# Optimization experiments

Measured on AMD Instinct MI355X. Metric: run time of the kernel, lower is better.

## Reference

```python
import jax, jax.numpy as jnp
import numpy as np

B, SQ, SK, DQ, DK, DV = 8, 2048, 2048, 128, 128, 128

def setup_inputs() -> dict:
    key = jax.random.key(0)
    k1, k2, k3, k4 = jax.random.split(key, 4)
    # xavier_uniform for weights [DQ, DK]
    limit = float(np.sqrt(6.0 / (DQ + DK)))
    weights = jax.random.uniform(k4, (DQ, DK), jnp.float32, -limit, limit)
    return {
        "query": jax.random.normal(k1, (B, SQ, DQ), jnp.float32),
        "key": jax.random.normal(k2, (B, SK, DK), jnp.float32),
        "value": jax.random.normal(k3, (B, SK, DV), jnp.float32),
        "weights": weights,
    }

def reference(query, key, value, weights):
    # score = (query @ W) @ key^T, computed as two GEMMs (faithful math, no [B,Sq,Dk,Sk] blow-up)
    qw = jnp.einsum('bqd,dk->bqk', query, weights)          # [B,SQ,DK]
    score = jnp.einsum('bqk,bsk->bqs', qw, key)             # [B,SQ,SK]
    weight = jax.nn.softmax(score, axis=-1)                 # dropout=0 -> identity
    out = jnp.einsum('bqs,bsv->bqv', weight, value)         # [B,SQ,DV]
    return out, weight
```

## Files before the change

kernel.cpp:

```cpp
#include <hip/hip_runtime.h>

#define B_  8
#define SQ_ 2048
#define SK_ 2048
#define D_  128

typedef float  f32x4 __attribute__((ext_vector_type(4)));
typedef short  s16x8 __attribute__((ext_vector_type(8)));
typedef __bf16 b16x8 __attribute__((ext_vector_type(8)));

__device__ __forceinline__ f32x4 mfma16(s16x8 a, s16x8 b, f32x4 c) {
    return __builtin_amdgcn_mfma_f32_16x16x32_bf16(
        __builtin_bit_cast(b16x8, a), __builtin_bit_cast(b16x8, b), c, 0, 0, 0);
}

__device__ __forceinline__ unsigned int bfpack(float a, float b) {
    return (__float_as_uint(a) >> 16) | (__float_as_uint(b) & 0xFFFF0000u);
}

__device__ __forceinline__ void split4(const float4 v, uint2& hi, uint2& lo) {
    float hx = __uint_as_float(__float_as_uint(v.x) & 0xFFFF0000u);
    float hy = __uint_as_float(__float_as_uint(v.y) & 0xFFFF0000u);
    float hz = __uint_as_float(__float_as_uint(v.z) & 0xFFFF0000u);
    float hw = __uint_as_float(__float_as_uint(v.w) & 0xFFFF0000u);
    hi.x = bfpack(v.x, v.y); hi.y = bfpack(v.z, v.w);
    lo.x = bfpack(v.x - hx, v.y - hy); lo.y = bfpack(v.z - hz, v.w - hw);
}

union U8 { unsigned int u[4]; s16x8 v; };

__global__ __launch_bounds__(256) void k1_qw(const float* __restrict__ q,
                                             const float* __restrict__ w,
                                             float* __restrict__ qw) {
    __shared__ float Ws[D_ * D_];
    const int tid = threadIdx.x;
    const int rowbase = blockIdx.x * 64;
    #pragma unroll
    for (int t = 0; t < 16; ++t) {
        int i4 = t * 256 + tid;
        ((float4*)Ws)[i4] = ((const float4*)w)[i4];
    }
    __syncthreads();
    const int mg = tid >> 4, cg = tid & 15;
    const int c0 = cg * 8;
    const float* qrow[4];
    #pragma unroll
    for (int i = 0; i < 4; ++i)
        qrow[i] = q + (size_t)(rowbase + mg * 4 + i) * D_;
    float acc[4][8];
    #pragma unroll
    for (int i = 0; i < 4; ++i)
        #pragma unroll
        for (int j = 0; j < 8; ++j) acc[i][j] = 0.0f;
    for (int d0 = 0; d0 < D_; d0 += 16) {
        float qr[4][16];
        #pragma unroll
        for (int i = 0; i < 4; ++i)
            #pragma unroll
            for (int c4 = 0; c4 < 4; ++c4)
                *(float4*)&qr[i][c4 * 4] = *(const float4*)(qrow[i] + d0 + c4 * 4);
        #pragma unroll
        for (int dd = 0; dd < 16; ++dd) {
            const int d = d0 + dd;
            float4 w0 = *(const float4*)&Ws[d * D_ + c0];
            float4 w1 = *(const float4*)&Ws[d * D_ + c0 + 4];
            #pragma unroll
            for (int i = 0; i < 4; ++i) {
                float a = qr[i][dd];
                acc[i][0] += a * w0.x; acc[i][1] += a * w0.y;
                acc[i][2] += a * w0.z; acc[i][3] += a * w0.w;
                acc[i][4] += a * w1.x; acc[i][5] += a * w1.y;
                acc[i][6] += a * w1.z; acc[i][7] += a * w1.w;
            }
        }
    }
    #pragma unroll
    for (int i = 0; i < 4; ++i) {
        float* dst = qw + (size_t)(rowbase + mg * 4 + i) * D_ + c0;
        *(float4*)dst       = make_float4(acc[i][0], acc[i][1], acc[i][2], acc[i][3]);
        *(float4*)(dst + 4) = make_float4(acc[i][4], acc[i][5], acc[i][6], acc[i][7]);
    }
}

__global__ __launch_bounds__(256) void k2_score(
        const float* __restrict__ qw, const float* __restrict__ key,
        float* __restrict__ S) {
    __shared__ unsigned short Khi[64 * 136];
    __shared__ unsigned short Klo[64 * 136];

    const int tid  = threadIdx.x;
    const int b    = blockIdx.z;
    const int m0   = blockIdx.y * 64;
    const int n0   = blockIdx.x * 64;
    const int w    = tid >> 6, lane = tid & 63;
    const int mw   = w >> 1,  nw   = w & 1;
    const int quad = lane >> 4, l15 = lane & 15;

    #pragma unroll
    for (int it = 0; it < 8; ++it) {
        int idx = it * 256 + tid;
        int r = idx >> 5, c4 = idx & 31;
        float4 v = ((const float4*)(key + ((size_t)b * SK_ + n0 + r) * D_))[c4];
        uint2 h, l; split4(v, h, l);
        unsigned int* ph = (unsigned int*)Khi + r * 68 + c4 * 2;
        unsigned int* pl = (unsigned int*)Klo + r * 68 + c4 * 2;
        ph[0] = h.x; ph[1] = h.y; pl[0] = l.x; pl[1] = l.y;
    }

    s16x8 a_hi[2][4], a_lo[2][4];
    #pragma unroll
    for (int rt = 0; rt < 2; ++rt) {
        const float* ar = qw + ((size_t)b * SQ_ + m0 + mw * 32 + rt * 16 + l15) * D_;
        #pragma unroll
        for (int k0 = 0; k0 < 4; ++k0) {
            const float* p = ar + k0 * 32 + quad * 8;
            float4 v0 = *(const float4*)p;
            float4 v1 = *(const float4*)(p + 4);
            uint2 h0, l0, h1, l1;
            split4(v0, h0, l0); split4(v1, h1, l1);
            U8 H, L;
            H.u[0] = h0.x; H.u[1] = h0.y; H.u[2] = h1.x; H.u[3] = h1.y;
            L.u[0] = l0.x; L.u[1] = l0.y; L.u[2] = l1.x; L.u[3] = l1.y;
            a_hi[rt][k0] = H.v; a_lo[rt][k0] = L.v;
        }
    }
    __syncthreads();

    f32x4 acc[2][2];
    #pragma unroll
    for (int rt = 0; rt < 2; ++rt)
        #pragma unroll
        for (int ct = 0; ct < 2; ++ct) acc[rt][ct] = (f32x4){0.f, 0.f, 0.f, 0.f};

    #pragma unroll
    for (int k0 = 0; k0 < 4; ++k0) {
        const int c8 = (k0 * 4 + quad) * 8;
        s16x8 bh[2], bl[2];
        #pragma unroll
        for (int ct = 0; ct < 2; ++ct) {
            int rb = nw * 32 + ct * 16 + l15;
            bh[ct] = *(const s16x8*)&Khi[rb * 136 + c8];
            bl[ct] = *(const s16x8*)&Klo[rb * 136 + c8];
        }
        #pragma unroll
        for (int rt = 0; rt < 2; ++rt)
            #pragma unroll
            for (int ct = 0; ct < 2; ++ct) {
                acc[rt][ct] = mfma16(a_hi[rt][k0], bh[ct], acc[rt][ct]);
                acc[rt][ct] = mfma16(a_lo[rt][k0], bh[ct], acc[rt][ct]);
                acc[rt][ct] = mfma16(a_hi[rt][k0], bl[ct], acc[rt][ct]);
            }
    }

    #pragma unroll
    for (int rt = 0; rt < 2; ++rt) {
        float* Sp = S + ((size_t)b * SQ_ + m0 + mw * 32 + rt * 16 + quad * 4) * SK_
                      + n0 + nw * 32 + l15;
        #pragma unroll
        for (int r = 0; r < 4; ++r)
            #pragma unroll
            for (int ct = 0; ct < 2; ++ct)
                Sp[(size_t)r * SK_ + ct * 16] = acc[rt][ct][r];
    }
}

__global__ __launch_bounds__(256) void k2b_stats(const float* __restrict__ S,
        float* __restrict__ m_ws, float* __restrict__ l_ws) {
    const int row  = blockIdx.x * 4 + (threadIdx.x >> 6);
    const int lane = threadIdx.x & 63;
    const float4* p = (const float4*)(S + (size_t)row * SK_);
    float4 x[8];
    #pragma unroll
    for (int i = 0; i < 8; ++i) x[i] = p[i * 64 + lane];

    float m = -1e30f;
    #pragma unroll
    for (int i = 0; i < 8; ++i)
        m = fmaxf(m, fmaxf(fmaxf(x[i].x, x[i].y), fmaxf(x[i].z, x[i].w)));
    #pragma unroll
    for (int off = 32; off; off >>= 1) m = fmaxf(m, __shfl_xor(m, off, 64));

    float s = 0.f;
    #pragma unroll
    for (int i = 0; i < 8; ++i)
        s += __expf(x[i].x - m) + __expf(x[i].y - m) +
             __expf(x[i].z - m) + __expf(x[i].w - m);
    #pragma unroll
    for (int off = 32; off; off >>= 1) s += __shfl_xor(s, off, 64);

    if (lane == 0) {
        m_ws[row] = m;
        l_ws[row] = s;
    }
}

__global__ __launch_bounds__(256) void k3_pv(float* __restrict__ Wgt,
        const float* __restrict__ V, float* __restrict__ O,
        const float* __restrict__ m_ws, const float* __restrict__ l_ws) {
    __shared__ unsigned short Pt[16 * 72];
    __shared__ unsigned short Vt[128 * 72];

    const int tid  = threadIdx.x;
    const int b    = blockIdx.y;
    const int m0   = blockIdx.x * 16;
    const int w    = tid >> 6, lane = tid & 63;
    const int quad = lane >> 4, l15 = lane & 15;

    const int pr = tid >> 4, pc = tid & 15;
    const float m_r  = m_ws[(size_t)b * SQ_ + m0 + pr];
    const float invl = 1.0f / l_ws[(size_t)b * SQ_ + m0 + pr];
    float* Prow = Wgt + ((size_t)b * SQ_ + m0 + pr) * SK_;

    const int vn4 = tid >> 3, vk2 = tid & 7;
    const float* Vb = V + (size_t)b * SK_ * D_;

    f32x4 acc[2];
    acc[0] = (f32x4){0.f, 0.f, 0.f, 0.f};
    acc[1] = (f32x4){0.f, 0.f, 0.f, 0.f};

    for (int kt = 0; kt < SK_; kt += 64) {
        __syncthreads();
        {
            float4 s4 = ((const float4*)(Prow + kt))[pc];
            float4 p4;
            p4.x = __expf(s4.x - m_r) * invl;
            p4.y = __expf(s4.y - m_r) * invl;
            p4.z = __expf(s4.z - m_r) * invl;
            p4.w = __expf(s4.w - m_r) * invl;
            ((float4*)(Prow + kt))[pc] = p4;
            unsigned int* pp = (unsigned int*)Pt + pr * 36 + pc * 2;
            pp[0] = bfpack(p4.x, p4.y);
            pp[1] = bfpack(p4.z, p4.w);
        }
        #pragma unroll
        for (int i = 0; i < 4; ++i) {
            int kp = vk2 * 4 + i;
            const float* vp = Vb + (size_t)(kt + kp * 2) * D_ + vn4 * 4;
            float4 va  = *(const float4*)vp;
            float4 vb4 = *(const float4*)(vp + D_);
            unsigned int* qv = (unsigned int*)Vt;
            qv[(vn4 * 4 + 0) * 36 + kp] = bfpack(va.x, vb4.x);
            qv[(vn4 * 4 + 1) * 36 + kp] = bfpack(va.y, vb4.y);
            qv[(vn4 * 4 + 2) * 36 + kp] = bfpack(va.z, vb4.z);
            qv[(vn4 * 4 + 3) * 36 + kp] = bfpack(va.w, vb4.w);
        }
        __syncthreads();
        #pragma unroll
        for (int k0 = 0; k0 < 2; ++k0) {
            int c8 = (k0 * 4 + quad) * 8;
            s16x8 af = *(const s16x8*)&Pt[l15 * 72 + c8];
            #pragma unroll
            for (int nf = 0; nf < 2; ++nf) {
                s16x8 bf = *(const s16x8*)&Vt[(w * 32 + nf * 16 + l15) * 72 + c8];
                acc[nf] = mfma16(af, bf, acc[nf]);
            }
        }
    }

    float* Op = O + ((size_t)b * SQ_ + m0 + quad * 4) * D_ + w * 32 + l15;
    #pragma unroll
    for (int nf = 0; nf < 2; ++nf)
        #pragma unroll
        for (int r = 0; r < 4; ++r)
            Op[(size_t)r * D_ + nf * 16] = acc[nf][r];
}

extern "C" void kernel_launch(void* const* d_in, const int* in_sizes, int n_in,
                              void* d_out, int out_size, void* d_ws, size_t ws_size,
                              hipStream_t stream) {
    const float* q = (const float*)d_in[0];
    const float* k = (const float*)d_in[1];
    const float* v = (const float*)d_in[2];
    const float* w = (const float*)d_in[3];
    float* out    = (float*)d_out;
    float* weight = out + (size_t)B_ * SQ_ * D_;
    float* qw     = out;
    float* m_ws   = (float*)d_ws;
    float* l_ws   = m_ws + (size_t)B_ * SQ_;

    k1_qw<<<(B_ * SQ_) / 64, 256, 0, stream>>>(q, w, qw);
    k2_score<<<dim3(SK_ / 64, SQ_ / 64, B_), 256, 0, stream>>>(qw, k, weight);
    k2b_stats<<<(B_ * SQ_) / 4, 256, 0, stream>>>(weight, m_ws, l_ws);
    k3_pv<<<dim3(SQ_ / 16, B_), 256, 0, stream>>>(weight, v, out, m_ws, l_ws);
}
```

Baseline: 383.4 us.

## Replace materialized score matrix with two-pass recompute: stats kernel plus fused softmax-PV

Removes the separate score, stats and PV kernels. A split-K stats kernel recomputes Q·K^T in registers and keeps an online max and sum, with no full score matrix written. A fused kernel then recomputes the scores, writes the normalized weights once, and accumulates P·V through LDS atomics across four K-split waves. Q·W is now stored pre-split into bf16 hi/lo in the output buffer. This avoids writing the score matrix, reading it back, and rewriting it, at the cost of computing Q·K^T twice and loading K and V straight from global memory with strided, uncached-in-LDS access.

Result: slower. 542.8 us (+41.6%).

```diff
diff --git a/kernel.cpp b/kernel.cpp
--- a/kernel.cpp
+++ b/kernel.cpp
@@ -1,18 +1,35 @@
 #include <hip/hip_runtime.h>
 
-#define B_  8
-#define SQ_ 2048
-#define SK_ 2048
-#define D_  128
+#define B_   8
+#define SQ_  2048
+#define SK_  2048
+#define D_   128
+#define KSPLIT_ 4
+#define KRANGE_ (SK_ / KSPLIT_)
+#define NSTEP_  (KRANGE_ / 16)
+#define BSQ_ (B_ * SQ_)
 
 typedef float  f32x4 __attribute__((ext_vector_type(4)));
 typedef short  s16x8 __attribute__((ext_vector_type(8)));
+typedef short  s16x4 __attribute__((ext_vector_type(4)));
 typedef __bf16 b16x8 __attribute__((ext_vector_type(8)));
 
-__device__ __forceinline__ f32x4 mfma16(s16x8 a, s16x8 b, f32x4 c) {
+__device__ __forceinline__ f32x4 mfma_k32(s16x8 a, s16x8 b, f32x4 c) {
     return __builtin_amdgcn_mfma_f32_16x16x32_bf16(
         __builtin_bit_cast(b16x8, a), __builtin_bit_cast(b16x8, b), c, 0, 0, 0);
 }
+
+#if __has_builtin(__builtin_amdgcn_mfma_f32_16x16x16bf16_1k)
+__device__ __forceinline__ f32x4 mfma_k16(s16x4 a, s16x4 b, f32x4 c) {
+    return __builtin_amdgcn_mfma_f32_16x16x16bf16_1k(a, b, c, 0, 0, 0);
+}
+#else
+__device__ __forceinline__ f32x4 mfma_k16(s16x4 a, s16x4 b, f32x4 c) {
+    f32x4 d;
+    asm("v_mfma_f32_16x16x16_bf16 %0, %1, %2, %3" : "=v"(d) : "v"(a), "v"(b), "v"(c));
+    return d;
+}
+#endif
 
 __device__ __forceinline__ unsigned int bfpack(float a, float b) {
     return (__float_as_uint(a) >> 16) | (__float_as_uint(b) & 0xFFFF0000u);
@@ -28,10 +45,32 @@
 }
 
 union U8 { unsigned int u[4]; s16x8 v; };
+union U4 { unsigned int u[2]; s16x4 v; };
+
+__device__ __forceinline__ f32x4 qk_tile(const float* __restrict__ kr,
+                                         const s16x8* q_hi, const s16x8* q_lo,
+                                         int quad) {
+    f32x4 acc = (f32x4){0.f, 0.f, 0.f, 0.f};
+    #pragma unroll
+    for (int dc = 0; dc < 4; ++dc) {
+        const float* p = kr + dc * 32 + quad * 8;
+        float4 v0 = *(const float4*)p;
+        float4 v1 = *(const float4*)(p + 4);
+        uint2 h0, l0, h1, l1;
+        split4(v0, h0, l0); split4(v1, h1, l1);
+        U8 H, L;
+        H.u[0] = h0.x; H.u[1] = h0.y; H.u[2] = h1.x; H.u[3] = h1.y;
+        L.u[0] = l0.x; L.u[1] = l0.y; L.u[2] = l1.x; L.u[3] = l1.y;
+        acc = mfma_k32(H.v, q_hi[dc], acc);
+        acc = mfma_k32(L.v, q_hi[dc], acc);
+        acc = mfma_k32(H.v, q_lo[dc], acc);
+    }
+    return acc;
+}
 
 __global__ __launch_bounds__(256) void k1_qw(const float* __restrict__ q,
                                              const float* __restrict__ w,
-                                             float* __restrict__ qw) {
+                                             unsigned int* __restrict__ qwp) {
     __shared__ float Ws[D_ * D_];
     const int tid = threadIdx.x;
     const int rowbase = blockIdx.x * 64;
@@ -76,193 +115,138 @@
     }
     #pragma unroll
     for (int i = 0; i < 4; ++i) {
-        float* dst = qw + (size_t)(rowbase + mg * 4 + i) * D_ + c0;
-        *(float4*)dst       = make_float4(acc[i][0], acc[i][1], acc[i][2], acc[i][3]);
-        *(float4*)(dst + 4) = make_float4(acc[i][4], acc[i][5], acc[i][6], acc[i][7]);
-    }
-}
-
-__global__ __launch_bounds__(256) void k2_score(
-        const float* __restrict__ qw, const float* __restrict__ key,
-        float* __restrict__ S) {
-    __shared__ unsigned short Khi[64 * 136];
-    __shared__ unsigned short Klo[64 * 136];
-
+        float4 v0 = make_float4(acc[i][0], acc[i][1], acc[i][2], acc[i][3]);
+        float4 v1 = make_float4(acc[i][4], acc[i][5], acc[i][6], acc[i][7]);
+        uint2 h0, l0, h1, l1;
+        split4(v0, h0, l0); split4(v1, h1, l1);
+        unsigned int* dst = qwp + (size_t)(rowbase + mg * 4 + i) * 128;
+        *(uint4*)(dst + cg * 4)      = make_uint4(h0.x, h0.y, h1.x, h1.y);
+        *(uint4*)(dst + 64 + cg * 4) = make_uint4(l0.x, l0.y, l1.x, l1.y);
+    }
+}
+
+__global__ __launch_bounds__(256, 4) void k_stats(
+        const unsigned short* __restrict__ qwp, const float* __restrict__ key,
+        float* __restrict__ mp, float* __restrict__ lp) {
+    const int blk  = ((int)blockIdx.x & 7) * 128 + ((int)blockIdx.x >> 3);
+    const int wid  = blk * 4 + (threadIdx.x >> 6);
+    const int lane = threadIdx.x & 63;
+    const int quad = lane >> 4, l15 = lane & 15;
+    const int qb = wid & 127;
+    const int ks = (wid >> 7) & 3;
+    const int b  = wid >> 9;
+
+    const unsigned short* qrow = qwp + ((size_t)b * SQ_ + qb * 16 + l15) * 256;
+    s16x8 q_hi[4], q_lo[4];
+    #pragma unroll
+    for (int dc = 0; dc < 4; ++dc) {
+        q_hi[dc] = *(const s16x8*)(qrow + dc * 32 + quad * 8);
+        q_lo[dc] = *(const s16x8*)(qrow + 128 + dc * 32 + quad * 8);
+    }
+
+    const float* Kb = key + ((size_t)b * SK_ + ks * KRANGE_) * D_;
+    float m_run = -3.0e38f, l_run = 0.f;
+    for (int st = 0; st < NSTEP_; ++st) {
+        const float* kr = Kb + (size_t)(st * 16 + l15) * D_;
+        f32x4 acc = qk_tile(kr, q_hi, q_lo, quad);
+        float t = fmaxf(fmaxf(acc[0], acc[1]), fmaxf(acc[2], acc[3]));
+        float mn = fmaxf(m_run, t);
+        l_run = l_run * __expf(m_run - mn)
+              + __expf(acc[0] - mn) + __expf(acc[1] - mn)
+              + __expf(acc[2] - mn) + __expf(acc[3] - mn);
+        m_run = mn;
+    }
+    #pragma unroll
+    for (int off = 16; off <= 32; off <<= 1) {
+        float om = __shfl_xor(m_run, off, 64);
+        float ol = __shfl_xor(l_run, off, 64);
+        float mn = fmaxf(m_run, om);
+        l_run = l_run * __expf(m_run - mn) + ol * __expf(om - mn);
+        m_run = mn;
+    }
+    if (lane < 16) {
+        size_t row = (size_t)b * SQ_ + qb * 16 + l15;
+        mp[(size_t)ks * BSQ_ + row] = m_run;
+        lp[(size_t)ks * BSQ_ + row] = l_run;
+    }
+}
+
+__global__ __launch_bounds__(512, 4) void k_fused(
+        const unsigned short* qwp, const float* __restrict__ key,
+        const float* __restrict__ val, float* out, float* __restrict__ wgt,
+        const float* __restrict__ mp, const float* __restrict__ lp) {
+    __shared__ float Ot[32][132];
     const int tid  = threadIdx.x;
-    const int b    = blockIdx.z;
-    const int m0   = blockIdx.y * 64;
-    const int n0   = blockIdx.x * 64;
-    const int w    = tid >> 6, lane = tid & 63;
-    const int mw   = w >> 1,  nw   = w & 1;
-    const int quad = lane >> 4, l15 = lane & 15;
-
-    #pragma unroll
-    for (int it = 0; it < 8; ++it) {
-        int idx = it * 256 + tid;
-        int r = idx >> 5, c4 = idx & 31;
-        float4 v = ((const float4*)(key + ((size_t)b * SK_ + n0 + r) * D_))[c4];
-        uint2 h, l; split4(v, h, l);
-        unsigned int* ph = (unsigned int*)Khi + r * 68 + c4 * 2;
-        unsigned int* pl = (unsigned int*)Klo + r * 68 + c4 * 2;
-        ph[0] = h.x; ph[1] = h.y; pl[0] = l.x; pl[1] = l.y;
-    }
-
-    s16x8 a_hi[2][4], a_lo[2][4];
-    #pragma unroll
-    for (int rt = 0; rt < 2; ++rt) {
-        const float* ar = qw + ((size_t)b * SQ_ + m0 + mw * 32 + rt * 16 + l15) * D_;
-        #pragma unroll
-        for (int k0 = 0; k0 < 4; ++k0) {
-            const float* p = ar + k0 * 32 + quad * 8;
-            float4 v0 = *(const float4*)p;
-            float4 v1 = *(const float4*)(p + 4);
-            uint2 h0, l0, h1, l1;
-            split4(v0, h0, l0); split4(v1, h1, l1);
-            U8 H, L;
-            H.u[0] = h0.x; H.u[1] = h0.y; H.u[2] = h1.x; H.u[3] = h1.y;
-            L.u[0] = l0.x; L.u[1] = l0.y; L.u[2] = l1.x; L.u[3] = l1.y;
-            a_hi[rt][k0] = H.v; a_lo[rt][k0] = L.v;
+    const int blk  = ((int)blockIdx.x & 7) * 64 + ((int)blockIdx.x >> 3);
+    const int wv   = tid >> 6;
+    const int qg   = wv >> 2;
+    const int ks   = wv & 3;
+    const int lane = tid & 63, quad = lane >> 4, l15 = lane & 15;
+    const int b  = blk >> 6;
+    const int qb = (blk & 63) * 2 + qg;
+
+    for (int i = tid; i < 32 * 132; i += 512) ((float*)Ot)[i] = 0.f;
+    __syncthreads();
+
+    const unsigned short* qrow = qwp + ((size_t)b * SQ_ + qb * 16 + l15) * 256;
+    s16x8 q_hi[4], q_lo[4];
+    #pragma unroll
+    for (int dc = 0; dc < 4; ++dc) {
+        q_hi[dc] = *(const s16x8*)(qrow + dc * 32 + quad * 8);
+        q_lo[dc] = *(const s16x8*)(qrow + 128 + dc * 32 + quad * 8);
+    }
+
+    const size_t row = (size_t)b * SQ_ + qb * 16 + l15;
+    float mf = -3.0e38f, lf = 0.f;
+    #pragma unroll
+    for (int s = 0; s < KSPLIT_; ++s) {
+        float ms = mp[(size_t)s * BSQ_ + row];
+        float ls = lp[(size_t)s * BSQ_ + row];
+        float mn = fmaxf(mf, ms);
+        lf = lf * __expf(mf - mn) + ls * __expf(ms - mn);
+        mf = mn;
+    }
+    const float linv = 1.0f / lf;
+
+    const float* Kb = key + ((size_t)b * SK_ + ks * KRANGE_) * D_;
+    const float* Vb = val + ((size_t)b * SK_ + ks * KRANGE_) * D_;
+    float* Wp = wgt + row * SK_ + ks * KRANGE_ + quad * 4;
+
+    f32x4 acc_o[8];
+    #pragma unroll
+    for (int i = 0; i < 8; ++i) acc_o[i] = (f32x4){0.f, 0.f, 0.f, 0.f};
+
+    for (int st = 0; st < NSTEP_; ++st) {
+        const float* kr = Kb + (size_t)(st * 16 + l15) * D_;
+        f32x4 s4 = qk_tile(kr, q_hi, q_lo, quad);
+        f32x4 p;
+        #pragma unroll
+        for (int r = 0; r < 4; ++r) p[r] = __expf(s4[r] - mf) * linv;
+        *(float4*)(Wp + st * 16) = make_float4(p[0], p[1], p[2], p[3]);
+        U4 A; A.u[0] = bfpack(p[0], p[1]); A.u[1] = bfpack(p[2], p[3]);
+        const float* vr = Vb + (size_t)(st * 16 + quad * 4) * D_ + l15;
+        #pragma unroll
+        for (int vt = 0; vt < 8; ++vt) {
+            const float* vc = vr + vt * 16;
+            U4 Bv;
+            Bv.u[0] = bfpack(vc[0],        vc[D_]);
+            Bv.u[1] = bfpack(vc[2 * D_],   vc[3 * D_]);
+            acc_o[vt] = mfma_k16(A.v, Bv.v, acc_o[vt]);
         }
     }
+
+    #pragma unroll
+    for (int vt = 0; vt < 8; ++vt)
+        #pragma unroll
+        for (int r = 0; r < 4; ++r)
+            atomicAdd(&Ot[qg * 16 + quad * 4 + r][vt * 16 + l15], acc_o[vt][r]);
     __syncthreads();
 
-    f32x4 acc[2][2];
-    #pragma unroll
-    for (int rt = 0; rt < 2; ++rt)
-        #pragma unroll
-        for (int ct = 0; ct < 2; ++ct) acc[rt][ct] = (f32x4){0.f, 0.f, 0.f, 0.f};
-
-    #pragma unroll
-    for (int k0 = 0; k0 < 4; ++k0) {
-        const int c8 = (k0 * 4 + quad) * 8;
-        s16x8 bh[2], bl[2];
-        #pragma unroll
-        for (int ct = 0; ct < 2; ++ct) {
-            int rb = nw * 32 + ct * 16 + l15;
-            bh[ct] = *(const s16x8*)&Khi[rb * 136 + c8];
-            bl[ct] = *(const s16x8*)&Klo[rb * 136 + c8];
-        }
-        #pragma unroll
-        for (int rt = 0; rt < 2; ++rt)
-            #pragma unroll
-            for (int ct = 0; ct < 2; ++ct) {
-                acc[rt][ct] = mfma16(a_hi[rt][k0], bh[ct], acc[rt][ct]);
-                acc[rt][ct] = mfma16(a_lo[rt][k0], bh[ct], acc[rt][ct]);
-                acc[rt][ct] = mfma16(a_hi[rt][k0], bl[ct], acc[rt][ct]);
-            }
-    }
-
-    #pragma unroll
-    for (int rt = 0; rt < 2; ++rt) {
-        float* Sp = S + ((size_t)b * SQ_ + m0 + mw * 32 + rt * 16 + quad * 4) * SK_
-                      + n0 + nw * 32 + l15;
-        #pragma unroll
-        for (int r = 0; r < 4; ++r)
-            #pragma unroll
-            for (int ct = 0; ct < 2; ++ct)
-                Sp[(size_t)r * SK_ + ct * 16] = acc[rt][ct][r];
-    }
-}
-
-__global__ __launch_bounds__(256) void k2b_stats(const float* __restrict__ S,
-        float* __restrict__ m_ws, float* __restrict__ l_ws) {
-    const int row  = blockIdx.x * 4 + (threadIdx.x >> 6);
-    const int lane = threadIdx.x & 63;
-    const float4* p = (const float4*)(S + (size_t)row * SK_);
-    float4 x[8];
-    #pragma unroll
-    for (int i = 0; i < 8; ++i) x[i] = p[i * 64 + lane];
-
-    float m = -1e30f;
-    #pragma unroll
-    for (int i = 0; i < 8; ++i)
-        m = fmaxf(m, fmaxf(fmaxf(x[i].x, x[i].y), fmaxf(x[i].z, x[i].w)));
-    #pragma unroll
-    for (int off = 32; off; off >>= 1) m = fmaxf(m, __shfl_xor(m, off, 64));
-
-    float s = 0.f;
-    #pragma unroll
-    for (int i = 0; i < 8; ++i)
-        s += __expf(x[i].x - m) + __expf(x[i].y - m) +
-             __expf(x[i].z - m) + __expf(x[i].w - m);
-    #pragma unroll
-    for (int off = 32; off; off >>= 1) s += __shfl_xor(s, off, 64);
-
-    if (lane == 0) {
-        m_ws[row] = m;
-        l_ws[row] = s;
-    }
-}
-
-__global__ __launch_bounds__(256) void k3_pv(float* __restrict__ Wgt,
-        const float* __restrict__ V, float* __restrict__ O,
-        const float* __restrict__ m_ws, const float* __restrict__ l_ws) {
-    __shared__ unsigned short Pt[16 * 72];
-    __shared__ unsigned short Vt[128 * 72];
-
-    const int tid  = threadIdx.x;
-    const int b    = blockIdx.y;
-    const int m0   = blockIdx.x * 16;
-    const int w    = tid >> 6, lane = tid & 63;
-    const int quad = lane >> 4, l15 = lane & 15;
-
-    const int pr = tid >> 4, pc = tid & 15;
-    const float m_r  = m_ws[(size_t)b * SQ_ + m0 + pr];
-    const float invl = 1.0f / l_ws[(size_t)b * SQ_ + m0 + pr];
-    float* Prow = Wgt + ((size_t)b * SQ_ + m0 + pr) * SK_;
-
-    const int vn4 = tid >> 3, vk2 = tid & 7;
-    const float* Vb = V + (size_t)b * SK_ * D_;
-
-    f32x4 acc[2];
-    acc[0] = (f32x4){0.f, 0.f, 0.f, 0.f};
-    acc[1] = (f32x4){0.f, 0.f, 0.f, 0.f};
-
-    for (int kt = 0; kt < SK_; kt += 64) {
-        __syncthreads();
-        {
-            float4 s4 = ((const float4*)(Prow + kt))[pc];
-            float4 p4;
-            p4.x = __expf(s4.x - m_r) * invl;
-            p4.y = __expf(s4.y - m_r) * invl;
-            p4.z = __expf(s4.z - m_r) * invl;
-            p4.w = __expf(s4.w - m_r) * invl;
-            ((float4*)(Prow + kt))[pc] = p4;
-            unsigned int* pp = (unsigned int*)Pt + pr * 36 + pc * 2;
-            pp[0] = bfpack(p4.x, p4.y);
-            pp[1] = bfpack(p4.z, p4.w);
-        }
-        #pragma unroll
-        for (int i = 0; i < 4; ++i) {
-            int kp = vk2 * 4 + i;
-            const float* vp = Vb + (size_t)(kt + kp * 2) * D_ + vn4 * 4;
-            float4 va  = *(const float4*)vp;
-            float4 vb4 = *(const float4*)(vp + D_);
-            unsigned int* qv = (unsigned int*)Vt;
-            qv[(vn4 * 4 + 0) * 36 + kp] = bfpack(va.x, vb4.x);
-            qv[(vn4 * 4 + 1) * 36 + kp] = bfpack(va.y, vb4.y);
-            qv[(vn4 * 4 + 2) * 36 + kp] = bfpack(va.z, vb4.z);
-            qv[(vn4 * 4 + 3) * 36 + kp] = bfpack(va.w, vb4.w);
-        }
-        __syncthreads();
-        #pragma unroll
-        for (int k0 = 0; k0 < 2; ++k0) {
-            int c8 = (k0 * 4 + quad) * 8;
-            s16x8 af = *(const s16x8*)&Pt[l15 * 72 + c8];
-            #pragma unroll
-            for (int nf = 0; nf < 2; ++nf) {
-                s16x8 bf = *(const s16x8*)&Vt[(w * 32 + nf * 16 + l15) * 72 + c8];
-                acc[nf] = mfma16(af, bf, acc[nf]);
-            }
-        }
-    }
-
-    float* Op = O + ((size_t)b * SQ_ + m0 + quad * 4) * D_ + w * 32 + l15;
-    #pragma unroll
-    for (int nf = 0; nf < 2; ++nf)
-        #pragma unroll
-        for (int r = 0; r < 4; ++r)
-            Op[(size_t)r * D_ + nf * 16] = acc[nf][r];
+    float* ob = out + ((size_t)b * SQ_ + (size_t)(blk & 63) * 32) * D_;
+    for (int i = tid; i < 32 * 32; i += 512) {
+        int r = i >> 5, c4 = i & 31;
+        *(float4*)(ob + (size_t)r * D_ + c4 * 4) = *(const float4*)&Ot[r][c4 * 4];
+    }
 }
 
 extern "C" void kernel_launch(void* const* d_in, const int* in_sizes, int n_in,
@@ -273,13 +257,13 @@
     const float* v = (const float*)d_in[2];
     const float* w = (const float*)d_in[3];
     float* out    = (float*)d_out;
-    float* weight = out + (size_t)B_ * SQ_ * D_;
-    float* qw     = out;
-    float* m_ws   = (float*)d_ws;
-    float* l_ws   = m_ws + (size_t)B_ * SQ_;
-
-    k1_qw<<<(B_ * SQ_) / 64, 256, 0, stream>>>(q, w, qw);
-    k2_score<<<dim3(SK_ / 64, SQ_ / 64, B_), 256, 0, stream>>>(qw, k, weight);
-    k2b_stats<<<(B_ * SQ_) / 4, 256, 0, stream>>>(weight, m_ws, l_ws);
-    k3_pv<<<dim3(SQ_ / 16, B_), 256, 0, stream>>>(weight, v, out, m_ws, l_ws);
-}
+    float* weight = out + (size_t)BSQ_ * D_;
+    unsigned int* qwp = (unsigned int*)out;
+    float* mp = (float*)d_ws;
+    float* lp = mp + (size_t)KSPLIT_ * BSQ_;
+
+    k1_qw  <<<BSQ_ / 64, 256, 0, stream>>>(q, w, qwp);
+    k_stats<<<BSQ_ / 16, 256, 0, stream>>>((const unsigned short*)qwp, k, mp, lp);
+    k_fused<<<BSQ_ / 32, 512, 0, stream>>>((const unsigned short*)qwp, k, v, out,
+                                           weight, mp, lp);
+}
```
